# Optimization experiments

Hardware: AMD Instinct MI355X
Metric: run time of the kernel (lower is better)

The kernel has to match this reference:

```python
import jax, jax.numpy as jnp
import numpy as np

HEADS = 4
HEAD_DIM = 32
SCALE = HEAD_DIM ** (-0.5)


def setup_inputs() -> dict:
    key = jax.random.key(0)
    k1, k2, k3, k4 = jax.random.split(key, 4)
    x = jax.random.normal(k1, (32, 256, 64, 64), dtype=jnp.float32)
    # to_qkv: Conv2d(256 -> 3*heads*head_dim=384, kernel 1x1, bias=False)
    w_qkv = jax.random.normal(k2, (384, 256), dtype=jnp.float32) * 0.02
    # to_out: Conv2d(128 -> 256, kernel 1x1, bias=True)
    w_out = jax.random.normal(k3, (256, 128), dtype=jnp.float32) * 0.02
    b_out = jax.random.normal(k4, (256,), dtype=jnp.float32) * 0.02
    return {"x": x, "w_qkv": w_qkv, "w_out": w_out, "b_out": b_out}


def reference(x, w_qkv, w_out, b_out):
    b, c, H, W = x.shape
    n = H * W
    # 1x1 conv == channel matmul; produce (b, 3, heads, head_dim, n)
    qkv = jnp.einsum('oc,bchw->bohw', w_qkv, x).reshape(b, 3, HEADS, HEAD_DIM, n)
    q, k, v = qkv[:, 0], qkv[:, 1], qkv[:, 2]  # each (b, h, d, n)
    q = jax.nn.softmax(q, axis=-1) * SCALE     # softmax over spatial n
    k = jax.nn.softmax(k, axis=-2)             # softmax over channel d
    # context: (b, h, e, d) -- reduce over n
    context = jnp.einsum('bhen,bhdn->bhed', k, v)
    # out: (b, h, d, n)
    out = jnp.einsum('bhed,bhen->bhdn', context, q)
    out = out.reshape(b, HEADS * HEAD_DIM, H, W)
    # to_out 1x1 conv with bias
    return jnp.einsum('oc,bchw->bohw', w_out, out) + b_out[None, :, None, None]
```

## Files before the change

### kernel.cpp

```cpp
#include <hip/hip_runtime.h>
#include <hip/hip_bf16.h>

#define NTOK 4096
#define SCALE 0.17677669529663687f

#define SWZ(r) ((((r) >> 1) ^ ((r) >> 3)) & 3)

using f32x4 = __attribute__((ext_vector_type(4))) float;
using s16x8 = __attribute__((ext_vector_type(8))) short;

__device__ __forceinline__ ushort bf_rne(float f) {
  unsigned int u = __builtin_bit_cast(unsigned int, f);
  u += 0x7FFFu + ((u >> 16) & 1u);
  return (ushort)(u >> 16);
}
__device__ __forceinline__ unsigned int pk2(float a, float b) {
  __hip_bfloat162 h = __float22bfloat162_rn(make_float2(a, b));
  unsigned int u;
  __builtin_memcpy(&u, &h, 4);
  return u;
}
__device__ __forceinline__ void gl_lds16(const ushort* g, ushort* l) {
  __builtin_amdgcn_global_load_lds(
      (const __attribute__((address_space(1))) unsigned int*)g,
      (__attribute__((address_space(3))) unsigned int*)l, 16, 0, 0);
}

__global__ __launch_bounds__(256) void k_cvt_w(const float* __restrict__ w,
                                               ushort* __restrict__ wb) {
  const int i = blockIdx.x * 256 + threadIdx.x;
  const float4 v = reinterpret_cast<const float4*>(w)[i];
  ushort4 h;
  h.x = bf_rne(v.x); h.y = bf_rne(v.y); h.z = bf_rne(v.z); h.w = bf_rne(v.w);
  reinterpret_cast<ushort4*>(wb)[i] = h;
}

__global__ __launch_bounds__(256) void k_qkv_mfma(const float* __restrict__ x,
                                                  const ushort* __restrict__ wb,
                                                  ushort* __restrict__ Ecn,
                                                  ushort* __restrict__ kb,
                                                  ushort* __restrict__ vb,
                                                  float* __restrict__ spart) {
  const int n0 = blockIdx.x * 128;
  const int b  = blockIdx.y;
  const float* xb = x + (size_t)b * 256 * NTOK;

  __shared__ ushort Bs[128 * 256];

  const int t = threadIdx.x;
  const int lane = t & 63;
  const int wv = t >> 6;
  const int wr = wv >> 1, wc = wv & 1;
  const int lm = lane & 15;
  const int lk = lane >> 4;

#pragma unroll
  for (int i = 0; i < 16; ++i) {
    const int u = t + 256 * i;
    const int n = u & 127;
    const int coct = u >> 7;
    const float* gp = xb + (size_t)(coct * 8) * NTOK + n0 + n;
    union { s16x8 v; unsigned int w[4]; } pk;
#pragma unroll
    for (int j = 0; j < 4; ++j)
      pk.w[j] = pk2(gp[(size_t)(2 * j) * NTOK], gp[(size_t)(2 * j + 1) * NTOK]);
    *reinterpret_cast<s16x8*>(Bs + n * 256 + 8 * (coct ^ (n & 7))) = pk.v;
  }
  __syncthreads();

  int brow[4];
#pragma unroll
  for (int nf = 0; nf < 4; ++nf) brow[nf] = wc * 64 + nf * 16 + lm;

#pragma unroll
  for (int y = 0; y < 3; ++y) {
    const int o0 = y * 128;
    const ushort* abase[4];
#pragma unroll
    for (int mf = 0; mf < 4; ++mf)
      abase[mf] = wb + (size_t)(o0 + wr * 64 + mf * 16 + lm) * 256 + lk * 8;

    f32x4 acc[4][4];
#pragma unroll
    for (int i = 0; i < 4; ++i)
#pragma unroll
      for (int j = 0; j < 4; ++j) acc[i][j] = (f32x4){0.f, 0.f, 0.f, 0.f};

#pragma unroll
    for (int it = 0; it < 8; ++it) {
      s16x8 af[4], bf[4];
#pragma unroll
      for (int mf = 0; mf < 4; ++mf)
        af[mf] = *reinterpret_cast<const s16x8*>(abase[mf] + it * 32);
#pragma unroll
      for (int nf = 0; nf < 4; ++nf) {
        const int cc = it * 4 + lk;
        bf[nf] = *reinterpret_cast<const s16x8*>(
            Bs + brow[nf] * 256 + 8 * (cc ^ (brow[nf] & 7)));
      }
#pragma unroll
      for (int mf = 0; mf < 4; ++mf)
#pragma unroll
        for (int nf = 0; nf < 4; ++nf)
          acc[mf][nf] = __builtin_amdgcn_mfma_f32_16x16x32_bf16(af[mf], bf[nf], acc[mf][nf], 0, 0, 0);
    }

    if (y == 0) {
      ushort* C = Ecn + (size_t)b * 128 * NTOK + n0;
      float* sp = spart + (((size_t)b * 32 + blockIdx.x) * 2 + wc) * 128;
#pragma unroll
      for (int mf = 0; mf < 4; ++mf) {
#pragma unroll
        for (int r = 0; r < 4; ++r) {
          const int ch = wr * 64 + mf * 16 + lk * 4 + r;
          float s = 0.f;
#pragma unroll
          for (int nf = 0; nf < 4; ++nf) {
            const float e = __expf(acc[mf][nf][r]);
            s += e;
            C[(size_t)ch * NTOK + wc * 64 + nf * 16 + lm] = bf_rne(e);
          }
          s += __shfl_xor(s, 1, 64);
          s += __shfl_xor(s, 2, 64);
          s += __shfl_xor(s, 4, 64);
          s += __shfl_xor(s, 8, 64);
          if (lm == 0) sp[ch] = s;
        }
      }
    } else if (y == 1) {
#pragma unroll
      for (int nf = 0; nf < 4; ++nf) {
#pragma unroll
        for (int g = 0; g < 2; ++g) {
          float m = -1e30f;
#pragma unroll
          for (int mm = 0; mm < 2; ++mm)
#pragma unroll
            for (int r = 0; r < 4; ++r)
              m = fmaxf(m, acc[g * 2 + mm][nf][r]);
          m = fmaxf(m, __shfl_xor(m, 16, 64));
          m = fmaxf(m, __shfl_xor(m, 32, 64));
          float s = 0.f;
#pragma unroll
          for (int mm = 0; mm < 2; ++mm)
#pragma unroll
            for (int r = 0; r < 4; ++r) {
              const float e = __expf(acc[g * 2 + mm][nf][r] - m);
              acc[g * 2 + mm][nf][r] = e;
              s += e;
            }
          s += __shfl_xor(s, 16, 64);
          s += __shfl_xor(s, 32, 64);
          const float inv = 1.0f / s;
#pragma unroll
          for (int mm = 0; mm < 2; ++mm)
#pragma unroll
            for (int r = 0; r < 4; ++r) acc[g * 2 + mm][nf][r] *= inv;
        }
      }
      ushort* C = kb + (size_t)b * 128 * NTOK + n0;
#pragma unroll
      for (int mf = 0; mf < 4; ++mf) {
        const int row0 = wr * 64 + mf * 16 + lk * 4;
#pragma unroll
        for (int nf = 0; nf < 4; ++nf) {
          const int col = wc * 64 + nf * 16 + lm;
#pragma unroll
          for (int r = 0; r < 4; ++r)
            C[(size_t)(row0 + r) * NTOK + col] = bf_rne(acc[mf][nf][r]);
        }
      }
    } else {
      ushort* C = vb + (size_t)b * 128 * NTOK + n0;
#pragma unroll
      for (int mf = 0; mf < 4; ++mf) {
        const int row0 = wr * 64 + mf * 16 + lk * 4;
#pragma unroll
        for (int nf = 0; nf < 4; ++nf) {
          const int col = wc * 64 + nf * 16 + lm;
#pragma unroll
          for (int r = 0; r < 4; ++r)
            C[(size_t)(row0 + r) * NTOK + col] = bf_rne(acc[mf][nf][r]);
        }
      }
    }
  }
}

__global__ __launch_bounds__(256) void k_context_mfma(const ushort* __restrict__ kb,
                                                      const ushort* __restrict__ vb,
                                                      float* __restrict__ ctx_part) {
  const int bh = blockIdx.x;
  const int w = threadIdx.x >> 6;
  const int lane = threadIdx.x & 63;
  const int lm = lane & 15, lk = lane >> 4;
  const ushort* kp = kb + (size_t)bh * 32 * NTOK + (size_t)w * 1024;
  const ushort* vp = vb + (size_t)bh * 32 * NTOK + (size_t)w * 1024;
  f32x4 acc[2][2];
#pragma unroll
  for (int i = 0; i < 2; ++i)
#pragma unroll
    for (int j = 0; j < 2; ++j) acc[i][j] = (f32x4){0.f, 0.f, 0.f, 0.f};
#pragma unroll 4
  for (int ks = 0; ks < 32; ++ks) {
    const int coff = ks * 32 + lk * 8;
    const s16x8 a0 = *reinterpret_cast<const s16x8*>(kp + (size_t)lm * NTOK + coff);
    const s16x8 a1 = *reinterpret_cast<const s16x8*>(kp + (size_t)(16 + lm) * NTOK + coff);
    const s16x8 b0 = *reinterpret_cast<const s16x8*>(vp + (size_t)lm * NTOK + coff);
    const s16x8 b1 = *reinterpret_cast<const s16x8*>(vp + (size_t)(16 + lm) * NTOK + coff);
    acc[0][0] = __builtin_amdgcn_mfma_f32_16x16x32_bf16(a0, b0, acc[0][0], 0, 0, 0);
    acc[0][1] = __builtin_amdgcn_mfma_f32_16x16x32_bf16(a0, b1, acc[0][1], 0, 0, 0);
    acc[1][0] = __builtin_amdgcn_mfma_f32_16x16x32_bf16(a1, b0, acc[1][0], 0, 0, 0);
    acc[1][1] = __builtin_amdgcn_mfma_f32_16x16x32_bf16(a1, b1, acc[1][1], 0, 0, 0);
  }
  float* op = ctx_part + ((size_t)bh * 4 + w) * 1024;
#pragma unroll
  for (int et = 0; et < 2; ++et)
#pragma unroll
    for (int dt = 0; dt < 2; ++dt)
#pragma unroll
      for (int r = 0; r < 4; ++r)
        op[(et * 16 + lk * 4 + r) * 32 + dt * 16 + lm] = acc[et][dt][r];
}

__global__ __launch_bounds__(256) void k_w2(const float* __restrict__ ctx_part,
                                            const float* __restrict__ spart,
                                            const float* __restrict__ w_out,
                                            ushort* __restrict__ W2b) {
  const int b = blockIdx.x;
  const int t = threadIdx.x;
  __shared__ float ctx[4096];
  __shared__ float fbuf[128];
#pragma unroll
  for (int i = 0; i < 16; ++i) {
    const int idx = t + 256 * i;
    const int h = idx >> 10, ed = idx & 1023;
    const float* cp = ctx_part + ((size_t)((b * 4 + h) * 4)) * 1024 + ed;
    ctx[idx] = cp[0] + cp[1024] + cp[2048] + cp[3072];
  }
  if (t < 128) {
    float s = 0.f;
    for (int p = 0; p < 64; ++p) s += spart[((size_t)b * 64 + p) * 128 + t];
    fbuf[t] = SCALE / s;
  }
  __syncthreads();
  const float* wrow = w_out + (size_t)t * 128;
  ushort* wout_row = W2b + ((size_t)b * 256 + t) * 128;
  float wv[32];
  for (int h = 0; h < 4; ++h) {
#pragma unroll
    for (int d = 0; d < 32; ++d) wv[d] = wrow[h * 32 + d];
#pragma unroll 4
    for (int e = 0; e < 32; ++e) {
      float a = 0.f;
#pragma unroll
      for (int d = 0; d < 32; ++d) a += wv[d] * ctx[h * 1024 + e * 32 + d];
      wout_row[h * 32 + e] = bf_rne(a * fbuf[h * 32 + e]);
    }
  }
}

__global__ __launch_bounds__(256) void k_out_mfma(const ushort* __restrict__ Ecn,
                                                  const ushort* __restrict__ W2b,
                                                  const float* __restrict__ b_out,
                                                  float* __restrict__ out) {
  const int n0 = blockIdx.x * 128;
  const int o0 = blockIdx.y * 128;
  const int b  = blockIdx.z;
  const ushort* A  = W2b + (size_t)b * 256 * 128;
  const ushort* Bq = Ecn + (size_t)b * 128 * NTOK;

  __shared__ ushort As[8192];
  __shared__ ushort Bt[8192];

  const int t = threadIdx.x;
  const int lane = t & 63;
  const int wv = t >> 6;
  const int wr = wv >> 1, wc = wv & 1;
  const int lm = lane & 15;
  const int lk = lane >> 4;

  int aoff[4][2], boff[4][2];
#pragma unroll
  for (int mf = 0; mf < 4; ++mf) {
    const int ar = wr * 64 + mf * 16 + lm;
#pragma unroll
    for (int ks = 0; ks < 2; ++ks)
      aoff[mf][ks] = ar * 64 + 8 * ((ks * 4 + lk) ^ (ar & 7));
  }
#pragma unroll
  for (int nf = 0; nf < 4; ++nf) {
    const int br = wc * 64 + nf * 16 + lm;
#pragma unroll
    for (int ks = 0; ks < 2; ++ks)
      boff[nf][ks] = br * 64 + 8 * ((ks * 4 + lk) ^ (br & 7));
  }
  size_t gaA[4];
  int lb[4];
#pragma unroll
  for (int i = 0; i < 4; ++i) {
    const int s_total = t + 256 * i;
    const int r = s_total >> 3;
    const int q = (s_total & 7) ^ (r & 7);
    gaA[i] = (size_t)(o0 + r) * 128 + q * 8;
    lb[i] = wv * 512 + i * 2048;
  }
  int bst[8], bn[8], bcg[8];
#pragma unroll
  for (int i = 0; i < 8; ++i) {
    const int u = t + 256 * i;
    bn[i] = u & 127;
    bcg[i] = u >> 7;
    bst[i] = bn[i] * 64 + 8 * ((bcg[i] >> 1) ^ (bn[i] & 7)) + (bcg[i] & 1) * 4;
  }

  f32x4 acc[4][4];
#pragma unroll
  for (int i = 0; i < 4; ++i)
#pragma unroll
    for (int j = 0; j < 4; ++j) acc[i][j] = (f32x4){0.f, 0.f, 0.f, 0.f};

  for (int it = 0; it < 2; ++it) {
    const size_t c0 = (size_t)it * 64;
    __syncthreads();
#pragma unroll
    for (int i = 0; i < 4; ++i)
      gl_lds16(A + gaA[i] + c0, As + lb[i]);
#pragma unroll
    for (int i = 0; i < 8; ++i) {
      const ushort* gp = Bq + (c0 + bcg[i] * 4) * NTOK + n0 + bn[i];
      ushort4 hvec;
      hvec.x = gp[0];
      hvec.y = gp[NTOK];
      hvec.z = gp[2 * NTOK];
      hvec.w = gp[3 * NTOK];
      *reinterpret_cast<ushort4*>(Bt + bst[i]) = hvec;
    }
    __syncthreads();
#pragma unroll
    for (int ks = 0; ks < 2; ++ks) {
      s16x8 af[4], bf[4];
#pragma unroll
      for (int mf = 0; mf < 4; ++mf)
        af[mf] = *reinterpret_cast<const s16x8*>(As + aoff[mf][ks]);
#pragma unroll
      for (int nf = 0; nf < 4; ++nf)
        bf[nf] = *reinterpret_cast<const s16x8*>(Bt + boff[nf][ks]);
#pragma unroll
      for (int mf = 0; mf < 4; ++mf)
#pragma unroll
        for (int nf = 0; nf < 4; ++nf)
          acc[mf][nf] = __builtin_amdgcn_mfma_f32_16x16x32_bf16(af[mf], bf[nf], acc[mf][nf], 0, 0, 0);
    }
  }

  float* C = out + ((size_t)b * 256 + o0) * NTOK + n0;
#pragma unroll
  for (int mf = 0; mf < 4; ++mf) {
    const int row0 = wr * 64 + mf * 16 + lk * 4;
#pragma unroll
    for (int nf = 0; nf < 4; ++nf) {
      const int col = wc * 64 + nf * 16 + lm;
#pragma unroll
      for (int r = 0; r < 4; ++r) {
        const float bias = b_out[o0 + row0 + r];
        C[(size_t)(row0 + r) * NTOK + col] = acc[mf][nf][r] + bias;
      }
    }
  }
}

extern "C" void kernel_launch(void* const* d_in, const int* in_sizes, int n_in,
                              void* d_out, int out_size, void* d_ws, size_t ws_size,
                              hipStream_t stream) {
  const float* x     = (const float*)d_in[0];
  const float* w_qkv = (const float*)d_in[1];
  const float* w_out = (const float*)d_in[2];
  const float* b_out = (const float*)d_in[3];
  float* out = (float*)d_out;

  ushort* kb  = (ushort*)d_ws;
  ushort* vb  = kb + (size_t)16777216;
  ushort* Ecn = vb + (size_t)16777216;
  float*  ctx_part = (float*)(Ecn + (size_t)16777216);
  float*  spart    = ctx_part + 524288;
  ushort* wb  = (ushort*)(spart + 262144);
  ushort* W2b = wb + 98304;

  k_cvt_w<<<96, 256, 0, stream>>>(w_qkv, wb);
  k_qkv_mfma<<<dim3(32, 32), 256, 0, stream>>>(x, wb, Ecn, kb, vb, spart);
  k_context_mfma<<<128, 256, 0, stream>>>(kb, vb, ctx_part);
  k_w2<<<32, 256, 0, stream>>>(ctx_part, spart, w_out, W2b);
  k_out_mfma<<<dim3(32, 2, 32), 256, 0, stream>>>(Ecn, W2b, b_out, out);
}
```

Baseline: 180.0 us.

## Halve QKV and context tile sizes to double grid parallelism, prefetch weight fragments

The QKV projection kernel now processes 64 tokens per block instead of 128, halving LDS use (64KB to 32KB) and accumulator registers, which doubles the grid to 2048 blocks. The intent is more resident blocks per CU and better latency hiding. Weight fragments are software-prefetched one k-step ahead. The context kernel splits each head's token range across 8 segments instead of 4, doubling its grid, and the partial-sum buffers and reduction in k_w2 are enlarged to match. In exchange, each weight fragment is reused across fewer token columns, so weights are reloaded more often, and the reduction pass has more partials to sum.

```diff
diff --git a/kernel.cpp b/kernel.cpp
--- a/kernel.cpp
+++ b/kernel.cpp
@@ -41,11 +41,11 @@
                                                   ushort* __restrict__ kb,
                                                   ushort* __restrict__ vb,
                                                   float* __restrict__ spart) {
-  const int n0 = blockIdx.x * 128;
+  const int n0 = blockIdx.x * 64;
   const int b  = blockIdx.y;
   const float* xb = x + (size_t)b * 256 * NTOK;
 
-  __shared__ ushort Bs[128 * 256];
+  __shared__ ushort Bs[64 * 256];
 
   const int t = threadIdx.x;
   const int lane = t & 63;
@@ -55,10 +55,10 @@
   const int lk = lane >> 4;
 
 #pragma unroll
-  for (int i = 0; i < 16; ++i) {
+  for (int i = 0; i < 8; ++i) {
     const int u = t + 256 * i;
-    const int n = u & 127;
-    const int coct = u >> 7;
+    const int n = u & 63;
+    const int coct = u >> 6;
     const float* gp = xb + (size_t)(coct * 8) * NTOK + n0 + n;
     union { s16x8 v; unsigned int w[4]; } pk;
 #pragma unroll
@@ -68,9 +68,9 @@
   }
   __syncthreads();
 
-  int brow[4];
-#pragma unroll
-  for (int nf = 0; nf < 4; ++nf) brow[nf] = wc * 64 + nf * 16 + lm;
+  int brow[2];
+#pragma unroll
+  for (int nf = 0; nf < 2; ++nf) brow[nf] = wc * 32 + nf * 16 + lm;
 
 #pragma unroll
   for (int y = 0; y < 3; ++y) {
@@ -80,20 +80,28 @@
     for (int mf = 0; mf < 4; ++mf)
       abase[mf] = wb + (size_t)(o0 + wr * 64 + mf * 16 + lm) * 256 + lk * 8;
 
-    f32x4 acc[4][4];
+    f32x4 acc[4][2];
 #pragma unroll
     for (int i = 0; i < 4; ++i)
 #pragma unroll
-      for (int j = 0; j < 4; ++j) acc[i][j] = (f32x4){0.f, 0.f, 0.f, 0.f};
+      for (int j = 0; j < 2; ++j) acc[i][j] = (f32x4){0.f, 0.f, 0.f, 0.f};
+
+    s16x8 afc[4];
+#pragma unroll
+    for (int mf = 0; mf < 4; ++mf)
+      afc[mf] = *reinterpret_cast<const s16x8*>(abase[mf]);
 
 #pragma unroll
     for (int it = 0; it < 8; ++it) {
-      s16x8 af[4], bf[4];
-#pragma unroll
-      for (int mf = 0; mf < 4; ++mf)
-        af[mf] = *reinterpret_cast<const s16x8*>(abase[mf] + it * 32);
-#pragma unroll
-      for (int nf = 0; nf < 4; ++nf) {
+      s16x8 afn[4];
+      if (it < 7) {
+#pragma unroll
+        for (int mf = 0; mf < 4; ++mf)
+          afn[mf] = *reinterpret_cast<const s16x8*>(abase[mf] + (it + 1) * 32);
+      }
+      s16x8 bf[2];
+#pragma unroll
+      for (int nf = 0; nf < 2; ++nf) {
         const int cc = it * 4 + lk;
         bf[nf] = *reinterpret_cast<const s16x8*>(
             Bs + brow[nf] * 256 + 8 * (cc ^ (brow[nf] & 7)));
@@ -101,13 +109,15 @@
 #pragma unroll
       for (int mf = 0; mf < 4; ++mf)
 #pragma unroll
-        for (int nf = 0; nf < 4; ++nf)
-          acc[mf][nf] = __builtin_amdgcn_mfma_f32_16x16x32_bf16(af[mf], bf[nf], acc[mf][nf], 0, 0, 0);
+        for (int nf = 0; nf < 2; ++nf)
+          acc[mf][nf] = __builtin_amdgcn_mfma_f32_16x16x32_bf16(afc[mf], bf[nf], acc[mf][nf], 0, 0, 0);
+#pragma unroll
+      for (int mf = 0; mf < 4; ++mf) afc[mf] = afn[mf];
     }
 
     if (y == 0) {
       ushort* C = Ecn + (size_t)b * 128 * NTOK + n0;
-      float* sp = spart + (((size_t)b * 32 + blockIdx.x) * 2 + wc) * 128;
+      float* sp = spart + (((size_t)b * 64 + blockIdx.x) * 2 + wc) * 128;
 #pragma unroll
       for (int mf = 0; mf < 4; ++mf) {
 #pragma unroll
@@ -115,10 +125,10 @@
           const int ch = wr * 64 + mf * 16 + lk * 4 + r;
           float s = 0.f;
 #pragma unroll
-          for (int nf = 0; nf < 4; ++nf) {
+          for (int nf = 0; nf < 2; ++nf) {
             const float e = __expf(acc[mf][nf][r]);
             s += e;
-            C[(size_t)ch * NTOK + wc * 64 + nf * 16 + lm] = bf_rne(e);
+            C[(size_t)ch * NTOK + wc * 32 + nf * 16 + lm] = bf_rne(e);
           }
           s += __shfl_xor(s, 1, 64);
           s += __shfl_xor(s, 2, 64);
@@ -129,7 +139,7 @@
       }
     } else if (y == 1) {
 #pragma unroll
-      for (int nf = 0; nf < 4; ++nf) {
+      for (int nf = 0; nf < 2; ++nf) {
 #pragma unroll
         for (int g = 0; g < 2; ++g) {
           float m = -1e30f;
@@ -163,8 +173,8 @@
       for (int mf = 0; mf < 4; ++mf) {
         const int row0 = wr * 64 + mf * 16 + lk * 4;
 #pragma unroll
-        for (int nf = 0; nf < 4; ++nf) {
-          const int col = wc * 64 + nf * 16 + lm;
+        for (int nf = 0; nf < 2; ++nf) {
+          const int col = wc * 32 + nf * 16 + lm;
 #pragma unroll
           for (int r = 0; r < 4; ++r)
             C[(size_t)(row0 + r) * NTOK + col] = bf_rne(acc[mf][nf][r]);
@@ -176,8 +186,8 @@
       for (int mf = 0; mf < 4; ++mf) {
         const int row0 = wr * 64 + mf * 16 + lk * 4;
 #pragma unroll
-        for (int nf = 0; nf < 4; ++nf) {
-          const int col = wc * 64 + nf * 16 + lm;
+        for (int nf = 0; nf < 2; ++nf) {
+          const int col = wc * 32 + nf * 16 + lm;
 #pragma unroll
           for (int r = 0; r < 4; ++r)
             C[(size_t)(row0 + r) * NTOK + col] = bf_rne(acc[mf][nf][r]);
@@ -190,19 +200,21 @@
 __global__ __launch_bounds__(256) void k_context_mfma(const ushort* __restrict__ kb,
                                                       const ushort* __restrict__ vb,
                                                       float* __restrict__ ctx_part) {
-  const int bh = blockIdx.x;
+  const int bh = blockIdx.x >> 1;
+  const int half = blockIdx.x & 1;
   const int w = threadIdx.x >> 6;
+  const int seg = half * 4 + w;
   const int lane = threadIdx.x & 63;
   const int lm = lane & 15, lk = lane >> 4;
-  const ushort* kp = kb + (size_t)bh * 32 * NTOK + (size_t)w * 1024;
-  const ushort* vp = vb + (size_t)bh * 32 * NTOK + (size_t)w * 1024;
+  const ushort* kp = kb + (size_t)bh * 32 * NTOK + (size_t)seg * 512;
+  const ushort* vp = vb + (size_t)bh * 32 * NTOK + (size_t)seg * 512;
   f32x4 acc[2][2];
 #pragma unroll
   for (int i = 0; i < 2; ++i)
 #pragma unroll
     for (int j = 0; j < 2; ++j) acc[i][j] = (f32x4){0.f, 0.f, 0.f, 0.f};
 #pragma unroll 4
-  for (int ks = 0; ks < 32; ++ks) {
+  for (int ks = 0; ks < 16; ++ks) {
     const int coff = ks * 32 + lk * 8;
     const s16x8 a0 = *reinterpret_cast<const s16x8*>(kp + (size_t)lm * NTOK + coff);
     const s16x8 a1 = *reinterpret_cast<const s16x8*>(kp + (size_t)(16 + lm) * NTOK + coff);
@@ -213,7 +225,7 @@
     acc[1][0] = __builtin_amdgcn_mfma_f32_16x16x32_bf16(a1, b0, acc[1][0], 0, 0, 0);
     acc[1][1] = __builtin_amdgcn_mfma_f32_16x16x32_bf16(a1, b1, acc[1][1], 0, 0, 0);
   }
-  float* op = ctx_part + ((size_t)bh * 4 + w) * 1024;
+  float* op = ctx_part + ((size_t)bh * 8 + seg) * 1024;
 #pragma unroll
   for (int et = 0; et < 2; ++et)
 #pragma unroll
@@ -235,12 +247,15 @@
   for (int i = 0; i < 16; ++i) {
     const int idx = t + 256 * i;
     const int h = idx >> 10, ed = idx & 1023;
-    const float* cp = ctx_part + ((size_t)((b * 4 + h) * 4)) * 1024 + ed;
-    ctx[idx] = cp[0] + cp[1024] + cp[2048] + cp[3072];
+    const float* cp = ctx_part + ((size_t)((b * 4 + h) * 8)) * 1024 + ed;
+    float a = 0.f;
+#pragma unroll
+    for (int j = 0; j < 8; ++j) a += cp[j * 1024];
+    ctx[idx] = a;
   }
   if (t < 128) {
     float s = 0.f;
-    for (int p = 0; p < 64; ++p) s += spart[((size_t)b * 64 + p) * 128 + t];
+    for (int p = 0; p < 128; ++p) s += spart[((size_t)b * 128 + p) * 128 + t];
     fbuf[t] = SCALE / s;
   }
   __syncthreads();
@@ -383,13 +398,13 @@
   ushort* vb  = kb + (size_t)16777216;
   ushort* Ecn = vb + (size_t)16777216;
   float*  ctx_part = (float*)(Ecn + (size_t)16777216);
-  float*  spart    = ctx_part + 524288;
-  ushort* wb  = (ushort*)(spart + 262144);
+  float*  spart    = ctx_part + 1048576;
+  ushort* wb  = (ushort*)(spart + 524288);
   ushort* W2b = wb + 98304;
 
   k_cvt_w<<<96, 256, 0, stream>>>(w_qkv, wb);
-  k_qkv_mfma<<<dim3(32, 32), 256, 0, stream>>>(x, wb, Ecn, kb, vb, spart);
-  k_context_mfma<<<128, 256, 0, stream>>>(kb, vb, ctx_part);
+  k_qkv_mfma<<<dim3(64, 32), 256, 0, stream>>>(x, wb, Ecn, kb, vb, spart);
+  k_context_mfma<<<256, 256, 0, stream>>>(kb, vb, ctx_part);
   k_w2<<<32, 256, 0, stream>>>(ctx_part, spart, w_out, W2b);
   k_out_mfma<<<dim3(32, 2, 32), 256, 0, stream>>>(Ecn, W2b, b_out, out);
 }
```

Result: slower. 216.4 us (+20.3%).
